# Optimization experiments

Measured on AMD Instinct MI355X. Metric: run time of the kernel, lower is better.

## Reference

```python
import jax, jax.numpy as jnp
import numpy as np

DIM = 512
HEADS = 16
WH, WW = 8, 8
B, NW = 8, 64
HD = DIM // HEADS            # 32, head dim
DR = HD // 2                 # 16, rotary dim per spatial axis
LN100 = float(np.log(100.0))


def _axial_freqs():
    # rotary-embedding-torch get_axial_freqs: per-axis freqs (interleaved repeat)
    inv = 1.0 / (10000.0 ** (np.arange(0, DR, 2, dtype=np.float32) / DR))  # (DR/2,)
    fh = np.repeat(np.arange(WH, dtype=np.float32)[:, None] * inv[None, :], 2, axis=-1)  # (WH, DR)
    fw = np.repeat(np.arange(WW, dtype=np.float32)[:, None] * inv[None, :], 2, axis=-1)  # (WW, DR)
    fh = np.broadcast_to(fh[:, None, :], (WH, WW, DR))
    fw = np.broadcast_to(fw[None, :, :], (WH, WW, DR))
    return jnp.asarray(np.concatenate([fh, fw], axis=-1))  # (WH, WW, HD)


def _rotate_half(t):
    # interleaved-pair rotation: (x0,x1) -> (-x1,x0)
    x = t.reshape(t.shape[:-1] + (t.shape[-1] // 2, 2))
    return jnp.stack([-x[..., 1], x[..., 0]], axis=-1).reshape(t.shape)


def _apply_rope(t, freqs):
    return t * jnp.cos(freqs) + _rotate_half(t) * jnp.sin(freqs)


def setup_inputs() -> dict:
    key = jax.random.key(0)
    k0, k1, k2 = jax.random.split(key, 3)
    x = jax.random.normal(k0, (B, NW, WH * WW, DIM), jnp.float32)
    qkv_weight = jax.random.normal(k1, (3 * DIM, DIM), jnp.float32) * 0.02
    q_bias = jnp.zeros((DIM,), jnp.float32)
    v_bias = jnp.zeros((DIM,), jnp.float32)
    logit_scale = jnp.full((HEADS, 1, 1, 1), float(np.log(10.0)), jnp.float32)
    proj_weight = jax.random.normal(k2, (DIM, DIM), jnp.float32) * 0.02
    proj_bias = jnp.zeros((DIM,), jnp.float32)
    return {"x": x, "qkv_weight": qkv_weight, "q_bias": q_bias, "v_bias": v_bias,
            "logit_scale": logit_scale, "proj_weight": proj_weight, "proj_bias": proj_bias}


def reference(x, qkv_weight, q_bias, v_bias, logit_scale, proj_weight, proj_bias):
    Bx, Nw, N, C = x.shape
    qkv_b = jnp.concatenate([q_bias, jnp.zeros_like(v_bias), v_bias])
    qkv = x @ qkv_weight.T + qkv_b                                   # (B, Nw, N, 3C)
    qkv = qkv.reshape(Bx, Nw, N, 3, HEADS, HD).transpose(3, 0, 4, 1, 2, 5)  # (3, B, H, Nw, N, hd)
    q, k, v = qkv[0], qkv[1], qkv[2]
    # cosine attention: L2-normalize q, k
    q = q / jnp.maximum(jnp.linalg.norm(q, axis=-1, keepdims=True), 1e-12)
    k = k / jnp.maximum(jnp.linalg.norm(k, axis=-1, keepdims=True), 1e-12)
    q = jnp.exp(jnp.clip(logit_scale, LN100, None)) * q             # per-head scale, clamp min=ln(100)
    # axial RoPE over the (Wh, Ww) window grid
    freqs = _axial_freqs()                                           # (WH, WW, HD)
    q = _apply_rope(q.reshape(Bx, HEADS, Nw, WH, WW, HD), freqs).reshape(Bx, HEADS, Nw, N, HD)
    k = _apply_rope(k.reshape(Bx, HEADS, Nw, WH, WW, HD), freqs).reshape(Bx, HEADS, Nw, N, HD)
    # block-diagonal (per-window) attention; flex_attention default scale 1/sqrt(hd)
    scores = jnp.einsum('bhwqd,bhwkd->bhwqk', q, k) * (1.0 / np.sqrt(HD))
    attn = jax.nn.softmax(scores, axis=-1)
    out = jnp.einsum('bhwqk,bhwkd->bhwqd', attn, v)                  # (B, H, Nw, N, hd)
    out = out.transpose(0, 2, 3, 1, 4).reshape(Bx, Nw, N, C)
    return out @ proj_weight.T + proj_bias
```

## Files before the change

### kernel.cpp

```cpp
#include <hip/hip_runtime.h>
#include <stdint.h>

#define DIMC   512
#define NHEADS 16
#define HDIM   32
#define NWIN   64
#define NTOK   64
#define NBATCH 8
#define MROWS  (NBATCH * NWIN * NTOK)

typedef unsigned short ushort_t;
typedef __attribute__((ext_vector_type(8))) short short8v;
typedef __attribute__((ext_vector_type(4))) float f32x4;

__device__ inline ushort_t f2bf(float f) {
    unsigned u = __float_as_uint(f);
    u += 0x7FFFu + ((u >> 16) & 1u);
    return (ushort_t)(u >> 16);
}
__device__ inline unsigned packbf2(float a, float b) {
    return ((unsigned)f2bf(a)) | (((unsigned)f2bf(b)) << 16);
}
__device__ inline void unpack8(uint4 u, float* f) {
    const unsigned a[4] = {u.x, u.y, u.z, u.w};
    #pragma unroll
    for (int j = 0; j < 4; ++j) {
        f[2*j+0] = __uint_as_float((a[j] & 0xFFFFu) << 16);
        f[2*j+1] = __uint_as_float(a[j] & 0xFFFF0000u);
    }
}

#define G2L16(gp, lp) __builtin_amdgcn_global_load_lds( \
    (const __attribute__((address_space(1))) unsigned int*)(gp), \
    (__attribute__((address_space(3))) unsigned int*)(lp), 16, 0, 0)

__global__ __launch_bounds__(256) void cvt_f32_bf16(
    const float* __restrict__ in, ushort_t* __restrict__ out, int n4)
{
    int i = blockIdx.x * 256 + threadIdx.x;
    if (i < n4) {
        float4 v = reinterpret_cast<const float4*>(in)[i];
        ushort4 o;
        o.x = f2bf(v.x); o.y = f2bf(v.y); o.z = f2bf(v.z); o.w = f2bf(v.w);
        reinterpret_cast<ushort4*>(out)[i] = o;
    }
}

__global__ void build_qkv_bias(const float* __restrict__ qb,
                               const float* __restrict__ vb,
                               float* __restrict__ bias)
{
    int i = blockIdx.x * 256 + threadIdx.x;
    if (i < 3 * DIMC) {
        float v = 0.f;
        if (i < DIMC) v = qb[i];
        else if (i >= 2 * DIMC) v = vb[i - 2 * DIMC];
        bias[i] = v;
    }
}

template<bool OUT_BF16>
__global__ __launch_bounds__(256) void gemm_bt_128x64(
    const ushort_t* __restrict__ A, const ushort_t* __restrict__ B,
    const float* __restrict__ bias, void* __restrict__ C,
    int M, int N, int K)
{
    __shared__ ushort_t lsA[128 * 64];
    __shared__ ushort_t lsB[128 * 64];

    const int tid = threadIdx.x;
    const int l   = tid & 63;
    const int wv  = tid >> 6;
    const int wr  = wv >> 1;
    const int wc  = wv & 1;
    const size_t mBase = (size_t)blockIdx.y * 128;
    const size_t nBase = (size_t)blockIdx.x * 128;

    f32x4 acc[4][4] = {};

    const int rl    = l >> 3;
    const int chunk = (l & 7) ^ rl;
    const ushort_t* gA0 = A + (mBase + (size_t)(wv * 32 + rl)) * (size_t)K + chunk * 8;
    const ushort_t* gB0 = B + (nBase + (size_t)(wv * 32 + rl)) * (size_t)K + chunk * 8;
    ushort_t* lA0 = &lsA[(wv * 32) * 64];
    ushort_t* lB0 = &lsB[(wv * 32) * 64];

    for (int k0 = 0; k0 < K; k0 += 64) {
        #pragma unroll
        for (int j = 0; j < 4; ++j) {
            G2L16(gA0 + (size_t)(j * 8) * (size_t)K + k0, lA0 + j * 8 * 64);
            G2L16(gB0 + (size_t)(j * 8) * (size_t)K + k0, lB0 + j * 8 * 64);
        }
        __syncthreads();

        #pragma unroll
        for (int kk = 0; kk < 2; ++kk) {
            short8v aF[4], bF[4];
            #pragma unroll
            for (int m = 0; m < 4; ++m) {
                const int row = wr * 64 + m * 16 + (l & 15);
                const int ps  = (kk * 4 + (l >> 4)) ^ (row & 7);
                aF[m] = *reinterpret_cast<const short8v*>(
                    reinterpret_cast<const char*>(lsA) + row * 128 + ps * 16);
            }
            #pragma unroll
            for (int n = 0; n < 4; ++n) {
                const int row = wc * 64 + n * 16 + (l & 15);
                const int ps  = (kk * 4 + (l >> 4)) ^ (row & 7);
                bF[n] = *reinterpret_cast<const short8v*>(
                    reinterpret_cast<const char*>(lsB) + row * 128 + ps * 16);
            }
            #pragma unroll
            for (int m = 0; m < 4; ++m)
                #pragma unroll
                for (int n = 0; n < 4; ++n)
                    acc[m][n] = __builtin_amdgcn_mfma_f32_16x16x32_bf16(
                        aF[m], bF[n], acc[m][n], 0, 0, 0);
        }
        __syncthreads();
    }

    const int c0 = l & 15;
    const int r0 = (l >> 4) * 4;
    #pragma unroll
    for (int m = 0; m < 4; ++m) {
        #pragma unroll
        for (int n = 0; n < 4; ++n) {
            const size_t gn = nBase + (size_t)(wc * 64 + n * 16 + c0);
            const float bv = bias[gn];
            #pragma unroll
            for (int i = 0; i < 4; ++i) {
                const size_t gm = mBase + (size_t)(wr * 64 + m * 16 + r0 + i);
                const float val = acc[m][n][i] + bv;
                if (OUT_BF16) ((ushort_t*)C)[gm * (size_t)N + gn] = f2bf(val);
                else          ((float*)C)  [gm * (size_t)N + gn] = val;
            }
        }
    }
}

__global__ __launch_bounds__(64, 3) void win_attn_mfma(
    const ushort_t* __restrict__ qkv,
    const float* __restrict__ logit_scale,
    ushort_t* __restrict__ attn_out)
{
    __shared__ __align__(16) ushort_t lsP[64 * 64];
    __shared__ __align__(16) ushort_t lsV[2 * 64 * 16];
    __shared__ float2 csT[8][8];

    const int l = threadIdx.x;
    const int c = l & 15;
    const int g = l >> 4;
    const int blk = blockIdx.x;
    const int w = blk & 63;
    const int h = (blk >> 6) & 15;
    const int b = blk >> 10;
    const size_t R = ((size_t)(b * 64 + w)) * 64;
    const ushort_t* qrow = qkv + R * 1536 + h * 32;

    {
        const ushort_t* vbase = qrow + 1024;
        #pragma unroll
        for (int half = 0; half < 2; ++half)
            #pragma unroll
            for (int kg = 0; kg < 2; ++kg) {
                const ushort_t* gsrc = vbase + (size_t)(kg * 32 + (l >> 1)) * 1536
                                       + half * 16 + (l & 1) * 8;
                G2L16(gsrc, &lsV[half * 1024 + kg * 512]);
            }
    }

    {
        const int pos = l >> 3, f = l & 7;
        const float inv = __expf(-(float)f * 1.1512925464970230f);
        const float ang = (float)pos * inv;
        csT[pos][f] = make_float2(__cosf(ang), __sinf(ang));
    }

    const float sc = __expf(fmaxf(logit_scale[h], 4.6051701859880914f))
                     * 0.17677669529663687f;

    short8v Qf[4], Kf[4];
    #pragma unroll
    for (int mi = 0; mi < 4; ++mi) {
        const int tok = mi * 16 + c;
        const ushort_t* qp = qrow + (size_t)tok * 1536 + g * 8;
        uint4 uq = *reinterpret_cast<const uint4*>(qp);
        uint4 uk = *reinterpret_cast<const uint4*>(qp + 512);
        float qv[8], kv[8];
        unpack8(uq, qv); unpack8(uk, kv);

        float sq = 0.f, sk = 0.f;
        #pragma unroll
        for (int d = 0; d < 8; ++d) { sq += qv[d] * qv[d]; sk += kv[d] * kv[d]; }
        sq += __shfl_xor(sq, 16); sq += __shfl_xor(sq, 32);
        sk += __shfl_xor(sk, 16); sk += __shfl_xor(sk, 32);
        const float qs = sc * rsqrtf(fmaxf(sq, 1e-24f));
        const float ks =      rsqrtf(fmaxf(sk, 1e-24f));

        const int wh = tok >> 3, ww = tok & 7;
        const int axpos = (g >= 2) ? ww : wh;
        union { short8v v; unsigned u[4]; } pq, pk2;
        #pragma unroll
        for (int pp = 0; pp < 4; ++pp) {
            const float2 cs = csT[axpos][(g & 1) * 4 + pp];
            float a0 = qv[2*pp] * qs, a1 = qv[2*pp+1] * qs;
            const float q0 = a0 * cs.x - a1 * cs.y;
            const float q1 = a1 * cs.x + a0 * cs.y;
            a0 = kv[2*pp] * ks; a1 = kv[2*pp+1] * ks;
            const float k0 = a0 * cs.x - a1 * cs.y;
            const float k1 = a1 * cs.x + a0 * cs.y;
            pq.u[pp]  = packbf2(q0, q1);
            pk2.u[pp] = packbf2(k0, k1);
        }
        Qf[mi] = pq.v; Kf[mi] = pk2.v;
    }

    f32x4 S[4][4];
    #pragma unroll
    for (int ki = 0; ki < 4; ++ki)
        #pragma unroll
        for (int qi = 0; qi < 4; ++qi)
            S[ki][qi] = __builtin_amdgcn_mfma_f32_16x16x32_bf16(
                Kf[ki], Qf[qi], (f32x4){0.f, 0.f, 0.f, 0.f}, 0, 0, 0);

    float isum[4];
    #pragma unroll
    for (int qi = 0; qi < 4; ++qi) {
        float m = -1e30f;
        #pragma unroll
        for (int ki = 0; ki < 4; ++ki)
            #pragma unroll
            for (int i = 0; i < 4; ++i) m = fmaxf(m, S[ki][qi][i]);
        m = fmaxf(m, __shfl_xor(m, 16));
        m = fmaxf(m, __shfl_xor(m, 32));
        float sum = 0.f;
        #pragma unroll
        for (int ki = 0; ki < 4; ++ki)
            #pragma unroll
            for (int i = 0; i < 4; ++i) {
                const float p = __expf(S[ki][qi][i] - m);
                S[ki][qi][i] = p; sum += p;
            }
        sum += __shfl_xor(sum, 16); sum += __shfl_xor(sum, 32);
        isum[qi] = 1.0f / sum;
    }

    #pragma unroll
    for (int qi = 0; qi < 4; ++qi) {
        const int q = qi * 16 + c;
        #pragma unroll
        for (int ki = 0; ki < 4; ++ki) {
            const int s2 = 2 * ki + (g >> 1);
            const int byteoff = q * 128 + ((s2 ^ (q & 7)) * 16) + (g & 1) * 8;
            uint2 pk2;
            pk2.x = packbf2(S[ki][qi][0], S[ki][qi][1]);
            pk2.y = packbf2(S[ki][qi][2], S[ki][qi][3]);
            *reinterpret_cast<uint2*>(reinterpret_cast<char*>(lsP) + byteoff) = pk2;
        }
    }

    asm volatile("s_waitcnt vmcnt(0)" ::: "memory");
    short8v Vf[2][2];
    #pragma unroll
    for (int half = 0; half < 2; ++half)
        #pragma unroll
        for (int ki = 0; ki < 2; ++ki) {
            union { short8v v; ushort_t e[8]; } t;
            #pragma unroll
            for (int j = 0; j < 8; ++j)
                t.e[j] = lsV[half * 1024 + (ki * 32 + g * 8 + j) * 16 + c];
            Vf[half][ki] = t.v;
        }

    short8v Pf[4][2];
    #pragma unroll
    for (int ni = 0; ni < 4; ++ni) {
        const int q = ni * 16 + c;
        #pragma unroll
        for (int ki = 0; ki < 2; ++ki) {
            const int s2 = ki * 4 + g;
            Pf[ni][ki] = *reinterpret_cast<const short8v*>(
                reinterpret_cast<const char*>(lsP) + q * 128 + ((s2 ^ (q & 7)) * 16));
        }
    }

    f32x4 O[2][4];
    #pragma unroll
    for (int mi = 0; mi < 2; ++mi)
        #pragma unroll
        for (int ni = 0; ni < 4; ++ni) {
            f32x4 a = __builtin_amdgcn_mfma_f32_16x16x32_bf16(
                Vf[mi][0], Pf[ni][0], (f32x4){0.f, 0.f, 0.f, 0.f}, 0, 0, 0);
            O[mi][ni] = __builtin_amdgcn_mfma_f32_16x16x32_bf16(
                Vf[mi][1], Pf[ni][1], a, 0, 0, 0);
        }

    #pragma unroll
    for (int ni = 0; ni < 4; ++ni) {
        const int q = ni * 16 + c;
        const float is = isum[ni];
        #pragma unroll
        for (int mi = 0; mi < 2; ++mi) {
            const int s = 2 * mi + (g >> 1);
            const int byteoff = q * 64 + ((s ^ (q & 3)) * 16) + (g & 1) * 8;
            uint2 pk2;
            pk2.x = packbf2(O[mi][ni][0] * is, O[mi][ni][1] * is);
            pk2.y = packbf2(O[mi][ni][2] * is, O[mi][ni][3] * is);
            *reinterpret_cast<uint2*>(reinterpret_cast<char*>(lsP) + byteoff) = pk2;
        }
    }

    const int qr0 = l >> 2, p = l & 3;
    ushort_t* obase = attn_out + R * 512 + h * 32;
    #pragma unroll
    for (int r = 0; r < 4; ++r) {
        const int q = qr0 + r * 16;
        uint4 row = *reinterpret_cast<const uint4*>(
            reinterpret_cast<const char*>(lsP) + q * 64 + ((p ^ (q & 3)) * 16));
        *reinterpret_cast<uint4*>(
            reinterpret_cast<char*>(obase + (size_t)q * 512) + p * 16) = row;
    }
}

extern "C" void kernel_launch(void* const* d_in, const int* in_sizes, int n_in,
                              void* d_out, int out_size, void* d_ws, size_t ws_size,
                              hipStream_t stream)
{
    (void)in_sizes; (void)n_in; (void)out_size; (void)ws_size;
    const float* x     = (const float*)d_in[0];
    const float* wqkv  = (const float*)d_in[1];
    const float* qb    = (const float*)d_in[2];
    const float* vb    = (const float*)d_in[3];
    const float* ls    = (const float*)d_in[4];
    const float* wproj = (const float*)d_in[5];
    const float* pb    = (const float*)d_in[6];
    float* out = (float*)d_out;

    char* ws = (char*)d_ws;
    ushort_t* xb      = (ushort_t*)(ws);
    ushort_t* wqkvb   = (ushort_t*)(ws + 33554432);
    ushort_t* wprojb  = (ushort_t*)(ws + 35127296);
    ushort_t* qkvb    = (ushort_t*)(ws + 35651584);
    ushort_t* attnb   = (ushort_t*)(ws + 136314880);
    float*    qkvbias = (float*)   (ws + 169869312);

    cvt_f32_bf16<<<16384, 256, 0, stream>>>(x,     xb,     16777216 / 4);
    cvt_f32_bf16<<<768,   256, 0, stream>>>(wqkv,  wqkvb,  786432   / 4);
    cvt_f32_bf16<<<256,   256, 0, stream>>>(wproj, wprojb, 262144   / 4);
    build_qkv_bias<<<6, 256, 0, stream>>>(qb, vb, qkvbias);

    gemm_bt_128x64<true><<<dim3(12, 256), 256, 0, stream>>>(
        xb, wqkvb, qkvbias, qkvb, MROWS, 3 * DIMC, DIMC);

    win_attn_mfma<<<NBATCH * NHEADS * NWIN, 64, 0, stream>>>(qkvb, ls, attnb);

    gemm_bt_128x64<false><<<dim3(4, 256), 256, 0, stream>>>(
        attnb, wprojb, pb, out, MROWS, DIMC, DIMC);
}
```

Before: 271.2 us.

## Double-buffer GEMM LDS tiles and swizzle block order across XCDs

The GEMM kernel now uses two LDS buffers, so the next K-tile is loaded while MFMAs run on the current one, with one barrier per iteration instead of two. Block indices are remapped with a swizzle over a 1D grid, which changes which tiles neighbouring workgroups handle and may improve L2 reuse on the multi-XCD part. An extra barrier is added in the attention kernel before LDS is reused for output. The cost is twice the LDS per block (64KB), which can lower occupancy.

```diff
diff --git a/kernel.cpp b/kernel.cpp
--- a/kernel.cpp
+++ b/kernel.cpp
@@ -60,21 +60,25 @@
 }
 
 template<bool OUT_BF16>
-__global__ __launch_bounds__(256) void gemm_bt_128x64(
+__global__ __launch_bounds__(256) void gemm_bt_2ph(
     const ushort_t* __restrict__ A, const ushort_t* __restrict__ B,
     const float* __restrict__ bias, void* __restrict__ C,
-    int M, int N, int K)
-{
-    __shared__ ushort_t lsA[128 * 64];
-    __shared__ ushort_t lsB[128 * 64];
+    int M, int N, int K, int nx)
+{
+    __shared__ ushort_t lsA[2][128 * 64];
+    __shared__ ushort_t lsB[2][128 * 64];
 
     const int tid = threadIdx.x;
     const int l   = tid & 63;
     const int wv  = tid >> 6;
     const int wr  = wv >> 1;
     const int wc  = wv & 1;
-    const size_t mBase = (size_t)blockIdx.y * 128;
-    const size_t nBase = (size_t)blockIdx.x * 128;
+
+    const int nwg = (int)gridDim.x;
+    const int bid = (int)blockIdx.x;
+    const int swz = (bid & 7) * (nwg >> 3) + (bid >> 3);
+    const size_t mBase = (size_t)(swz / nx) * 128;
+    const size_t nBase = (size_t)(swz % nx) * 128;
 
     f32x4 acc[4][4] = {};
 
@@ -82,17 +86,19 @@
     const int chunk = (l & 7) ^ rl;
     const ushort_t* gA0 = A + (mBase + (size_t)(wv * 32 + rl)) * (size_t)K + chunk * 8;
     const ushort_t* gB0 = B + (nBase + (size_t)(wv * 32 + rl)) * (size_t)K + chunk * 8;
-    ushort_t* lA0 = &lsA[(wv * 32) * 64];
-    ushort_t* lB0 = &lsB[(wv * 32) * 64];
-
-    for (int k0 = 0; k0 < K; k0 += 64) {
+
+    auto STAGE = [&](int buf, int t) {
+        const int k0 = t << 6;
         #pragma unroll
         for (int j = 0; j < 4; ++j) {
-            G2L16(gA0 + (size_t)(j * 8) * (size_t)K + k0, lA0 + j * 8 * 64);
-            G2L16(gB0 + (size_t)(j * 8) * (size_t)K + k0, lB0 + j * 8 * 64);
-        }
-        __syncthreads();
-
+            G2L16(gA0 + (size_t)(j * 8) * (size_t)K + k0,
+                  &lsA[buf][(wv * 32 + j * 8) * 64]);
+            G2L16(gB0 + (size_t)(j * 8) * (size_t)K + k0,
+                  &lsB[buf][(wv * 32 + j * 8) * 64]);
+        }
+    };
+
+    auto COMPUTE = [&](int buf) {
         #pragma unroll
         for (int kk = 0; kk < 2; ++kk) {
             short8v aF[4], bF[4];
@@ -101,14 +107,14 @@
                 const int row = wr * 64 + m * 16 + (l & 15);
                 const int ps  = (kk * 4 + (l >> 4)) ^ (row & 7);
                 aF[m] = *reinterpret_cast<const short8v*>(
-                    reinterpret_cast<const char*>(lsA) + row * 128 + ps * 16);
+                    reinterpret_cast<const char*>(lsA[buf]) + row * 128 + ps * 16);
             }
             #pragma unroll
             for (int n = 0; n < 4; ++n) {
                 const int row = wc * 64 + n * 16 + (l & 15);
                 const int ps  = (kk * 4 + (l >> 4)) ^ (row & 7);
                 bF[n] = *reinterpret_cast<const short8v*>(
-                    reinterpret_cast<const char*>(lsB) + row * 128 + ps * 16);
+                    reinterpret_cast<const char*>(lsB[buf]) + row * 128 + ps * 16);
             }
             #pragma unroll
             for (int m = 0; m < 4; ++m)
@@ -117,8 +123,19 @@
                     acc[m][n] = __builtin_amdgcn_mfma_f32_16x16x32_bf16(
                         aF[m], bF[n], acc[m][n], 0, 0, 0);
         }
+    };
+
+    const int nt = K >> 6;
+    STAGE(0, 0);
+    __syncthreads();
+    int cur = 0;
+    for (int t = 0; t < nt - 1; ++t) {
+        STAGE(cur ^ 1, t + 1);
+        COMPUTE(cur);
         __syncthreads();
-    }
+        cur ^= 1;
+    }
+    COMPUTE(cur);
 
     const int c0 = l & 15;
     const int r0 = (l >> 4) * 4;
@@ -296,6 +313,7 @@
                 Vf[mi][1], Pf[ni][1], a, 0, 0, 0);
         }
 
+    __syncthreads();
     #pragma unroll
     for (int ni = 0; ni < 4; ++ni) {
         const int q = ni * 16 + c;
@@ -350,11 +368,11 @@
     cvt_f32_bf16<<<256,   256, 0, stream>>>(wproj, wprojb, 262144   / 4);
     build_qkv_bias<<<6, 256, 0, stream>>>(qb, vb, qkvbias);
 
-    gemm_bt_128x64<true><<<dim3(12, 256), 256, 0, stream>>>(
-        xb, wqkvb, qkvbias, qkvb, MROWS, 3 * DIMC, DIMC);
+    gemm_bt_2ph<true><<<3072, 256, 0, stream>>>(
+        xb, wqkvb, qkvbias, qkvb, MROWS, 3 * DIMC, DIMC, 12);
 
     win_attn_mfma<<<NBATCH * NHEADS * NWIN, 64, 0, stream>>>(qkvb, ls, attnb);
 
-    gemm_bt_128x64<false><<<dim3(4, 256), 256, 0, stream>>>(
-        attnb, wprojb, pb, out, MROWS, DIMC, DIMC);
-}
+    gemm_bt_2ph<false><<<1024, 256, 0, stream>>>(
+        attnb, wprojb, pb, out, MROWS, DIMC, DIMC, 4);
+}
```

Result: faster. 259.9 us (-4.2%).
